# Optimization experiments

Measured on AMD Instinct MI355X. Metric: run time of the kernel, lower is better.

## Reference

```python
import jax, jax.numpy as jnp
import numpy as np

EPS = 1e-6
H = 64
SIGMA = 0.02


def setup_inputs() -> dict:
    key = jax.random.key(0)
    x = jax.random.normal(key, (8, 3, 65536), dtype=jnp.float32)
    return {"x": x}


def reference(x):
    # x: (B, 3, N) in roughly [-1, 1]; map to [0, 1]
    x = jnp.clip(x / 2.0 + 0.5, 0.0, 1.0)
    I = jnp.transpose(x, (0, 2, 1))  # (B, N, 3)
    # intensity scale I_y (intensity_scale=True)
    Iy = jnp.sqrt(jnp.sum(I * I, axis=-1, keepdims=True) + EPS)  # (B, N, 1)
    lin = jnp.linspace(-3.0, 3.0, H, dtype=I.dtype)  # (h,)
    logI = jnp.log(I + EPS)  # (B, N, 3)
    # log-chromaticity coordinates
    Iu = logI - logI[..., jnp.array([1, 0, 0])]  # (B, N, 3)
    Iv = logI - logI[..., jnp.array([2, 2, 1])]  # (B, N, 3)
    # inverse-quadratic kernel over bins: (B, N, 3, h)
    du = jnp.abs(Iu[..., None] - lin)
    dv = jnp.abs(Iv[..., None] - lin)
    ku = 1.0 / (1.0 + jnp.square(du) / (SIGMA ** 2))
    kv = 1.0 / (1.0 + jnp.square(dv) / (SIGMA ** 2))
    wu = Iy[..., None] * ku  # (B, N, 3, h)
    # reduce over pixels via batched outer product -> (B, 3, h, h)
    hists = jnp.einsum('bnch,bncg->bchg', wu, kv)
    return hists / (jnp.sum(hists, axis=(1, 2, 3), keepdims=True) + EPS)
```

## Files before the change

kernel.cpp:

```cpp
#include <hip/hip_runtime.h>
#include <hip/hip_bf16.h>


typedef __bf16 bf16x8 __attribute__((ext_vector_type(8)));
typedef float  f32x4  __attribute__((ext_vector_type(4)));

constexpr int   HBINS = 64;
constexpr float EPSF  = 1e-6f;
constexpr int   BATCH = 8;
constexpr int   NPIX  = 65536;
constexpr int   NBC   = 24;
constexpr int   CHUNKS = 32;
constexpr int   PPC   = NPIX / CHUNKS;
constexpr int   PITER = 256;
constexpr float BINSTEP  = 300.0f / 63.0f;
constexpr float LOGSCALE = 34.6573590279973f;

__global__ __launch_bounds__(256, 3) void hist_kernel(const float* __restrict__ x,
                                                      float* __restrict__ ws) {
    const int bc   = blockIdx.y;
    const int b    = bc / 3;
    const int c    = bc - b * 3;
    const int t    = threadIdx.x;
    const int lane = t & 63;
    const int w    = t >> 6;
    const int kgrp = lane >> 4;
    const int l16  = lane & 15;

    __shared__ float cu_s[PITER];
    __shared__ float cv_s[PITER];
    __shared__ float iy_s[PITER];
    __shared__ float lhist[HBINS * HBINS];

    for (int i = t; i < HBINS * HBINS; i += 256) lhist[i] = 0.0f;

    f32x4 acc[4][4];
#pragma unroll
    for (int m = 0; m < 4; ++m)
#pragma unroll
        for (int n = 0; n < 4; ++n) acc[m][n] = (f32x4){0.f, 0.f, 0.f, 0.f};

    const float* xr = x + ((size_t)b * 3 + 0) * NPIX;
    const float* xg = x + ((size_t)b * 3 + 1) * NPIX;
    const float* xb = x + ((size_t)b * 3 + 2) * NPIX;
    const int pix0 = blockIdx.x * PPC;

    for (int base = 0; base < PPC; base += PITER) {
        const int p = pix0 + base + t;
        float r  = xr[p], g = xg[p], bl = xb[p];
        r  = fminf(fmaxf(fmaf(r,  0.5f, 0.5f), 0.0f), 1.0f);
        g  = fminf(fmaxf(fmaf(g,  0.5f, 0.5f), 0.0f), 1.0f);
        bl = fminf(fmaxf(fmaf(bl, 0.5f, 0.5f), 0.0f), 1.0f);

        const float l2r = __log2f(r  + EPSF);
        const float l2g = __log2f(g  + EPSF);
        const float l2b = __log2f(bl + EPSF);

        float lc, lu, lv;
        if (c == 0)      { lc = l2r; lu = l2g; lv = l2b; }
        else if (c == 1) { lc = l2g; lu = l2r; lv = l2b; }
        else             { lc = l2b; lu = l2r; lv = l2g; }

        const float cu = (lc - lu) * LOGSCALE;
        const float cv = (lc - lv) * LOGSCALE;
        const float iy = __builtin_amdgcn_sqrtf(fmaf(r, r, fmaf(g, g, fmaf(bl, bl, EPSF))));

        __syncthreads();
        cu_s[t] = cu; cv_s[t] = cv; iy_s[t] = iy;
        __syncthreads();

#pragma unroll
        for (int ks = 0; ks < 2; ++ks) {
            const int k0 = w * 64 + ks * 32 + kgrp * 8;
            float cu8[8], cv8[8], iy8[8];
            *(float4*)&cu8[0] = *(const float4*)&cu_s[k0];
            *(float4*)&cu8[4] = *(const float4*)&cu_s[k0 + 4];
            *(float4*)&cv8[0] = *(const float4*)&cv_s[k0];
            *(float4*)&cv8[4] = *(const float4*)&cv_s[k0 + 4];
            *(float4*)&iy8[0] = *(const float4*)&iy_s[k0];
            *(float4*)&iy8[4] = *(const float4*)&iy_s[k0 + 4];

            bf16x8 bfr[4];
#pragma unroll
            for (int n = 0; n < 4; ++n) {
                const float ling = (float)(n * 16 + l16) * BINSTEP - 150.0f;
#pragma unroll
                for (int j = 0; j < 8; ++j) {
                    const float d = cv8[j] - ling;
                    bfr[n][j] = (__bf16)__builtin_amdgcn_rcpf(fmaf(d, d, 1.0f));
                }
            }
#pragma unroll
            for (int m = 0; m < 4; ++m) {
                const float linh = (float)(m * 16 + l16) * BINSTEP - 150.0f;
                bf16x8 af;
#pragma unroll
                for (int j = 0; j < 8; ++j) {
                    const float d = cu8[j] - linh;
                    af[j] = (__bf16)(iy8[j] * __builtin_amdgcn_rcpf(fmaf(d, d, 1.0f)));
                }
#pragma unroll
                for (int n = 0; n < 4; ++n)
                    acc[m][n] = __builtin_amdgcn_mfma_f32_16x16x32_bf16(af, bfr[n], acc[m][n], 0, 0, 0);
            }
        }
    }

    __syncthreads();
    const int crow = kgrp * 4;
#pragma unroll
    for (int m = 0; m < 4; ++m)
#pragma unroll
        for (int n = 0; n < 4; ++n)
#pragma unroll
            for (int ri = 0; ri < 4; ++ri)
                atomicAdd(&lhist[(m * 16 + crow + ri) * HBINS + n * 16 + l16], acc[m][n][ri]);
    __syncthreads();

    float* gh = ws + (size_t)bc * HBINS * HBINS;
    for (int i = t; i < HBINS * HBINS; i += 256) atomicAdd(&gh[i], lhist[i]);
}

__global__ __launch_bounds__(256) void norm_kernel(const float* __restrict__ ws,
                                                   float* __restrict__ out) {
    const int b = blockIdx.x;
    const float* h = ws  + (size_t)b * 3 * HBINS * HBINS;
    float*       o = out + (size_t)b * 3 * HBINS * HBINS;
    const int t = threadIdx.x;
    const int n = 3 * HBINS * HBINS;

    float s = 0.0f;
    for (int i = t; i < n; i += 256) s += h[i];
#pragma unroll
    for (int off = 32; off > 0; off >>= 1) s += __shfl_down(s, off, 64);

    __shared__ float partial[4];
    if ((t & 63) == 0) partial[t >> 6] = s;
    __syncthreads();
    const float total = partial[0] + partial[1] + partial[2] + partial[3];
    const float inv = 1.0f / (total + EPSF);

    for (int i = t; i < n; i += 256) o[i] = h[i] * inv;
}

extern "C" void kernel_launch(void* const* d_in, const int* in_sizes, int n_in,
                              void* d_out, int out_size, void* d_ws, size_t ws_size,
                              hipStream_t stream) {
    const float* x   = (const float*)d_in[0];
    float*       out = (float*)d_out;
    float*       ws  = (float*)d_ws;

    hipMemsetAsync(ws, 0, (size_t)NBC * HBINS * HBINS * sizeof(float), stream);

    dim3 grid(CHUNKS, NBC);
    hist_kernel<<<grid, 256, 0, stream>>>(x, ws);
    norm_kernel<<<BATCH, 256, 0, stream>>>(ws, out);
}
```

Before: 169.1 us.

## Give each wave its own pixel range and drop block barriers; double chunk count

Each wave now stages its own 64 pixels in a per-wave LDS slice and consumes them itself. This removes the two block-wide __syncthreads that every 256-pixel iteration needed before. The pixel chunk count per (batch, channel) doubles, giving more blocks to fill the GPU and fewer iterations per block. The cost is twice as many global atomic histogram flushes, and correctness now relies on in-order LDS access within a single wave.

```diff
diff --git a/kernel.cpp b/kernel.cpp
--- a/kernel.cpp
+++ b/kernel.cpp
@@ -10,9 +10,9 @@
 constexpr int   BATCH = 8;
 constexpr int   NPIX  = 65536;
 constexpr int   NBC   = 24;
-constexpr int   CHUNKS = 32;
+constexpr int   CHUNKS = 64;
 constexpr int   PPC   = NPIX / CHUNKS;
-constexpr int   PITER = 256;
+constexpr int   WPX   = PPC / 4;
 constexpr float BINSTEP  = 300.0f / 63.0f;
 constexpr float LOGSCALE = 34.6573590279973f;
 
@@ -27,9 +27,9 @@
     const int kgrp = lane >> 4;
     const int l16  = lane & 15;
 
-    __shared__ float cu_s[PITER];
-    __shared__ float cv_s[PITER];
-    __shared__ float iy_s[PITER];
+    __shared__ float cu_s[4][64];
+    __shared__ float cv_s[4][64];
+    __shared__ float iy_s[4][64];
     __shared__ float lhist[HBINS * HBINS];
 
     for (int i = t; i < HBINS * HBINS; i += 256) lhist[i] = 0.0f;
@@ -43,10 +43,10 @@
     const float* xr = x + ((size_t)b * 3 + 0) * NPIX;
     const float* xg = x + ((size_t)b * 3 + 1) * NPIX;
     const float* xb = x + ((size_t)b * 3 + 2) * NPIX;
-    const int pix0 = blockIdx.x * PPC;
+    const int wbase = blockIdx.x * PPC + w * WPX;
 
-    for (int base = 0; base < PPC; base += PITER) {
-        const int p = pix0 + base + t;
+    for (int it = 0; it < WPX; it += 64) {
+        const int p = wbase + it + lane;
         float r  = xr[p], g = xg[p], bl = xb[p];
         r  = fminf(fmaxf(fmaf(r,  0.5f, 0.5f), 0.0f), 1.0f);
         g  = fminf(fmaxf(fmaf(g,  0.5f, 0.5f), 0.0f), 1.0f);
@@ -61,24 +61,20 @@
         else if (c == 1) { lc = l2g; lu = l2r; lv = l2b; }
         else             { lc = l2b; lu = l2r; lv = l2g; }
 
-        const float cu = (lc - lu) * LOGSCALE;
-        const float cv = (lc - lv) * LOGSCALE;
-        const float iy = __builtin_amdgcn_sqrtf(fmaf(r, r, fmaf(g, g, fmaf(bl, bl, EPSF))));
-
-        __syncthreads();
-        cu_s[t] = cu; cv_s[t] = cv; iy_s[t] = iy;
-        __syncthreads();
+        cu_s[w][lane] = (lc - lu) * LOGSCALE;
+        cv_s[w][lane] = (lc - lv) * LOGSCALE;
+        iy_s[w][lane] = __builtin_amdgcn_sqrtf(fmaf(r, r, fmaf(g, g, fmaf(bl, bl, EPSF))));
 
 #pragma unroll
         for (int ks = 0; ks < 2; ++ks) {
-            const int k0 = w * 64 + ks * 32 + kgrp * 8;
+            const int k0 = ks * 32 + kgrp * 8;
             float cu8[8], cv8[8], iy8[8];
-            *(float4*)&cu8[0] = *(const float4*)&cu_s[k0];
-            *(float4*)&cu8[4] = *(const float4*)&cu_s[k0 + 4];
-            *(float4*)&cv8[0] = *(const float4*)&cv_s[k0];
-            *(float4*)&cv8[4] = *(const float4*)&cv_s[k0 + 4];
-            *(float4*)&iy8[0] = *(const float4*)&iy_s[k0];
-            *(float4*)&iy8[4] = *(const float4*)&iy_s[k0 + 4];
+            *(float4*)&cu8[0] = *(const float4*)&cu_s[w][k0];
+            *(float4*)&cu8[4] = *(const float4*)&cu_s[w][k0 + 4];
+            *(float4*)&cv8[0] = *(const float4*)&cv_s[w][k0];
+            *(float4*)&cv8[4] = *(const float4*)&cv_s[w][k0 + 4];
+            *(float4*)&iy8[0] = *(const float4*)&iy_s[w][k0];
+            *(float4*)&iy8[4] = *(const float4*)&iy_s[w][k0 + 4];
 
             bf16x8 bfr[4];
 #pragma unroll
```

New measurement: 229.0 us. 35.4% more time.

## Double-buffer per-pixel LDS staging and prefetch next pixel round

Applied to the files above, without the earlier changes.

The staging arrays in LDS become double-buffered. The global loads for the next 256 pixels are issued before the MFMA compute on the current buffer, and the log/sqrt preprocessing is written to the other buffer afterward. This removes one of the two barriers per iteration and hides global-load latency behind the kernel evaluation and MFMA work. In exchange it uses slightly more LDS and registers, which could affect occupancy at 3 blocks per CU.

```diff
diff --git a/kernel.cpp b/kernel.cpp
--- a/kernel.cpp
+++ b/kernel.cpp
@@ -12,7 +12,7 @@
 constexpr int   NBC   = 24;
 constexpr int   CHUNKS = 32;
 constexpr int   PPC   = NPIX / CHUNKS;
-constexpr int   PITER = 256;
+constexpr int   ROUNDS = PPC / 256;
 constexpr float BINSTEP  = 300.0f / 63.0f;
 constexpr float LOGSCALE = 34.6573590279973f;
 
@@ -27,9 +27,9 @@
     const int kgrp = lane >> 4;
     const int l16  = lane & 15;
 
-    __shared__ float cu_s[PITER];
-    __shared__ float cv_s[PITER];
-    __shared__ float iy_s[PITER];
+    __shared__ float cu_s[2][256];
+    __shared__ float cv_s[2][256];
+    __shared__ float iy_s[2][256];
     __shared__ float lhist[HBINS * HBINS];
 
     for (int i = t; i < HBINS * HBINS; i += 256) lhist[i] = 0.0f;
@@ -45,40 +45,50 @@
     const float* xb = x + ((size_t)b * 3 + 2) * NPIX;
     const int pix0 = blockIdx.x * PPC;
 
-    for (int base = 0; base < PPC; base += PITER) {
-        const int p = pix0 + base + t;
-        float r  = xr[p], g = xg[p], bl = xb[p];
+    auto produce = [&](float r, float g, float bl, float& cu, float& cv, float& iy) {
         r  = fminf(fmaxf(fmaf(r,  0.5f, 0.5f), 0.0f), 1.0f);
         g  = fminf(fmaxf(fmaf(g,  0.5f, 0.5f), 0.0f), 1.0f);
         bl = fminf(fmaxf(fmaf(bl, 0.5f, 0.5f), 0.0f), 1.0f);
-
         const float l2r = __log2f(r  + EPSF);
         const float l2g = __log2f(g  + EPSF);
         const float l2b = __log2f(bl + EPSF);
-
         float lc, lu, lv;
         if (c == 0)      { lc = l2r; lu = l2g; lv = l2b; }
         else if (c == 1) { lc = l2g; lu = l2r; lv = l2b; }
         else             { lc = l2b; lu = l2r; lv = l2g; }
+        cu = (lc - lu) * LOGSCALE;
+        cv = (lc - lv) * LOGSCALE;
+        iy = __builtin_amdgcn_sqrtf(fmaf(r, r, fmaf(g, g, fmaf(bl, bl, EPSF))));
+    };
 
-        const float cu = (lc - lu) * LOGSCALE;
-        const float cv = (lc - lv) * LOGSCALE;
-        const float iy = __builtin_amdgcn_sqrtf(fmaf(r, r, fmaf(g, g, fmaf(bl, bl, EPSF))));
+    {
+        float cu, cv, iy;
+        produce(xr[pix0 + t], xg[pix0 + t], xb[pix0 + t], cu, cv, iy);
+        cu_s[0][t] = cu; cv_s[0][t] = cv; iy_s[0][t] = iy;
+    }
+    __syncthreads();
 
-        __syncthreads();
-        cu_s[t] = cu; cv_s[t] = cv; iy_s[t] = iy;
-        __syncthreads();
+    for (int rnd = 0; rnd < ROUNDS; ++rnd) {
+        const int cur = rnd & 1;
+        const int nxt = cur ^ 1;
+        const bool have_next = (rnd + 1 < ROUNDS);
+
+        float rn = 0.f, gn = 0.f, bn = 0.f;
+        if (have_next) {
+            const int p = pix0 + (rnd + 1) * 256 + t;
+            rn = xr[p]; gn = xg[p]; bn = xb[p];
+        }
 
 #pragma unroll
         for (int ks = 0; ks < 2; ++ks) {
             const int k0 = w * 64 + ks * 32 + kgrp * 8;
             float cu8[8], cv8[8], iy8[8];
-            *(float4*)&cu8[0] = *(const float4*)&cu_s[k0];
-            *(float4*)&cu8[4] = *(const float4*)&cu_s[k0 + 4];
-            *(float4*)&cv8[0] = *(const float4*)&cv_s[k0];
-            *(float4*)&cv8[4] = *(const float4*)&cv_s[k0 + 4];
-            *(float4*)&iy8[0] = *(const float4*)&iy_s[k0];
-            *(float4*)&iy8[4] = *(const float4*)&iy_s[k0 + 4];
+            *(float4*)&cu8[0] = *(const float4*)&cu_s[cur][k0];
+            *(float4*)&cu8[4] = *(const float4*)&cu_s[cur][k0 + 4];
+            *(float4*)&cv8[0] = *(const float4*)&cv_s[cur][k0];
+            *(float4*)&cv8[4] = *(const float4*)&cv_s[cur][k0 + 4];
+            *(float4*)&iy8[0] = *(const float4*)&iy_s[cur][k0];
+            *(float4*)&iy8[4] = *(const float4*)&iy_s[cur][k0 + 4];
 
             bf16x8 bfr[4];
 #pragma unroll
@@ -104,9 +114,15 @@
                     acc[m][n] = __builtin_amdgcn_mfma_f32_16x16x32_bf16(af, bfr[n], acc[m][n], 0, 0, 0);
             }
         }
+
+        if (have_next) {
+            float cu, cv, iy;
+            produce(rn, gn, bn, cu, cv, iy);
+            cu_s[nxt][t] = cu; cv_s[nxt][t] = cv; iy_s[nxt][t] = iy;
+        }
+        __syncthreads();
     }
 
-    __syncthreads();
     const int crow = kgrp * 4;
 #pragma unroll
     for (int m = 0; m < 4; ++m)
```

Measured after the change: 169.7 us. No clear change (+0.3%).
